# Performance work log

Measured on AMD Instinct MI355X. Metric: run time of the kernel, lower is better.

## Reference

```python
import jax, jax.numpy as jnp
import numpy as np

N = 100000
IN_DIM = 256
HID = 64
HEADS = 2
OUT_DIM = 64
E = 1600000
NEG_SLOPE = 0.2


def gat_conv(x, edge_index, W, att_src, att_dst, bias):
    # PyG GATConv with heads=HEADS, concat=True, add_self_loops=True.
    # x: [N, IN_DIM]; edge_index: [2, E] (row0=src, row1=dst)
    loops = jnp.arange(N, dtype=edge_index.dtype)
    src = jnp.concatenate([edge_index[0], loops])  # [E+N]
    dst = jnp.concatenate([edge_index[1], loops])  # [E+N]
    h = (x @ W).reshape(N, HEADS, HID)             # [N, H, C]
    a_src = jnp.einsum('nhc,hc->nh', h, att_src)   # [N, H]
    a_dst = jnp.einsum('nhc,hc->nh', h, att_dst)   # [N, H]
    e = jax.nn.leaky_relu(a_src[src] + a_dst[dst], NEG_SLOPE)  # [E+N, H]
    # segment softmax over incoming edges of each dst node
    m = jax.ops.segment_max(e, dst, num_segments=N)            # [N, H]
    p = jnp.exp(e - m[dst])
    denom = jax.ops.segment_sum(p, dst, num_segments=N)        # [N, H]
    alpha = p / denom[dst]                                     # [E+N, H]
    msg = h[src] * alpha[:, :, None]                           # [E+N, H, C]
    out = jax.ops.segment_sum(msg, dst, num_segments=N)        # [N, H, C]
    return out.reshape(N, HEADS * HID) + bias


def setup_inputs() -> dict:
    key = jax.random.key(0)
    ks = jax.random.split(key, 12)
    s_in = 1.0 / np.sqrt(IN_DIM)
    s_h = 1.0 / np.sqrt(HID)
    s_fc = 1.0 / np.sqrt(HEADS * HID * 2)
    return {
        'x': jax.random.normal(ks[0], (N, IN_DIM), jnp.float32),
        'edge_index_connected': jax.random.randint(ks[1], (2, E), 0, N, jnp.int32),
        'edge_index_liked': jax.random.randint(ks[2], (2, E), 0, N, jnp.int32),
        'W1': jax.random.normal(ks[3], (IN_DIM, HEADS * HID), jnp.float32) * s_in,
        'att_src1': jax.random.normal(ks[4], (HEADS, HID), jnp.float32) * s_h,
        'att_dst1': jax.random.normal(ks[5], (HEADS, HID), jnp.float32) * s_h,
        'b1': jnp.zeros((HEADS * HID,), jnp.float32),
        'W2': jax.random.normal(ks[6], (IN_DIM, HEADS * HID), jnp.float32) * s_in,
        'att_src2': jax.random.normal(ks[7], (HEADS, HID), jnp.float32) * s_h,
        'att_dst2': jax.random.normal(ks[8], (HEADS, HID), jnp.float32) * s_h,
        'b2': jnp.zeros((HEADS * HID,), jnp.float32),
        'fc_W': jax.random.normal(ks[9], (HEADS * HID * 2, OUT_DIM), jnp.float32) * s_fc,
        'fc_b': jnp.zeros((OUT_DIM,), jnp.float32),
    }


def reference(x, edge_index_connected, edge_index_liked, W1, att_src1, att_dst1, b1,
              W2, att_src2, att_dst2, b2, fc_W, fc_b):
    xc = jax.nn.relu(gat_conv(x, edge_index_connected, W1, att_src1, att_dst1, b1))
    xl = jax.nn.relu(gat_conv(x, edge_index_liked, W2, att_src2, att_dst2, b2))
    x_comb = jnp.concatenate([xc, xl], axis=1)  # [N, 4*HID]
    return x_comb @ fc_W + fc_b
```

## Files before the change

### kernel.cpp

```cpp
#include <hip/hip_runtime.h>
#include <hip/hip_fp16.h>
#include <math.h>

#define NN 100000
#define IN_DIM 256
#define HCH 128
#define OUT_DIM 64
#define EE 1600000
#define NEG_SLOPE 0.2f

#define NB 1024
#define NPB 98
#define CAP 2048

typedef _Float16 half8v __attribute__((ext_vector_type(8)));
typedef _Float16 half4v __attribute__((ext_vector_type(4)));
typedef _Float16 half2v __attribute__((ext_vector_type(2)));
typedef float float4v __attribute__((ext_vector_type(4)));

__device__ __forceinline__ float lrelu(float v) { return v > 0.f ? v : NEG_SLOPE * v; }

__global__ void convw_kernel(const float* __restrict__ W0, const float* __restrict__ W1,
                             const float* __restrict__ fcW,
                             _Float16* __restrict__ wt, _Float16* __restrict__ fcw16)
{
    int i = blockIdx.x * 256 + threadIdx.x;
    if (i < 2 * IN_DIM * HCH) {
        int l = i >> 15, rem = i & 32767;
        int c = rem >> 8, k = rem & 255;
        const float* W = l ? W1 : W0;
        wt[i] = (_Float16)W[(size_t)k * HCH + c];
        return;
    }
    int j = i - 2 * IN_DIM * HCH;
    if (j < 2 * HCH * OUT_DIM) {
        int l = j >> 13, rem = j & 8191;
        int c = rem >> 7, k = rem & 127;
        fcw16[j] = (_Float16)fcW[(size_t)(l * HCH + k) * OUT_DIM + c];
    }
}

__global__ __launch_bounds__(256, 5) void gemm_mfma(
    const float* __restrict__ x, const _Float16* __restrict__ wt,
    const float* __restrict__ att_src, const float* __restrict__ att_dst,
    _Float16* __restrict__ h16, float* __restrict__ a_s, float* __restrict__ a_d, int n)
{
    __shared__ _Float16 smem[64 * 72 + 128 * 72];
    __shared__ float attv[2][128];
    _Float16 (*As)[72] = (_Float16(*)[72])smem;
    _Float16 (*Bs)[72] = (_Float16(*)[72])(smem + 64 * 72);
    const int tid = threadIdx.x;
    const int lane = tid & 63, wave = tid >> 6;
    const int wm = wave & 1, wn = wave >> 1;
    const int q = lane >> 4, r16 = lane & 15;
    const int row0 = blockIdx.x * 64;

    if (tid < 128) { attv[0][tid] = att_src[tid]; attv[1][tid] = att_dst[tid]; }

    float4v acc[2][4];
#pragma unroll
    for (int i = 0; i < 2; ++i)
#pragma unroll
        for (int j = 0; j < 4; ++j) acc[i][j] = (float4v){0.f, 0.f, 0.f, 0.f};

    const int ar = tid >> 2, aq = tid & 3;
    const int br = tid >> 1, bh = tid & 1;
    const bool rok = (row0 + ar) < n;
    for (int kt = 0; kt < IN_DIM; kt += 64) {
        const float* xp = x + (size_t)(row0 + ar) * IN_DIM + kt + aq * 16;
#pragma unroll
        for (int i = 0; i < 4; ++i) {
            float4 v = rok ? *(const float4*)(xp + i * 4) : make_float4(0.f, 0.f, 0.f, 0.f);
            half4v hv = { (_Float16)v.x, (_Float16)v.y, (_Float16)v.z, (_Float16)v.w };
            *(half4v*)&As[ar][aq * 16 + i * 4] = hv;
        }
        const _Float16* wp = wt + (size_t)br * IN_DIM + kt + bh * 32;
#pragma unroll
        for (int i = 0; i < 4; ++i)
            *(half8v*)&Bs[br][bh * 32 + i * 8] = *(const half8v*)(wp + i * 8);
        __syncthreads();
#pragma unroll
        for (int s = 0; s < 2; ++s) {
            half8v af[2], bf[4];
#pragma unroll
            for (int t = 0; t < 2; ++t)
                af[t] = *(half8v*)&As[wm * 32 + t * 16 + r16][s * 32 + q * 8];
#pragma unroll
            for (int t = 0; t < 4; ++t)
                bf[t] = *(half8v*)&Bs[wn * 64 + t * 16 + r16][s * 32 + q * 8];
#pragma unroll
            for (int mt = 0; mt < 2; ++mt)
#pragma unroll
                for (int nt = 0; nt < 4; ++nt)
                    acc[mt][nt] = __builtin_amdgcn_mfma_f32_16x16x32_f16(
                        af[mt], bf[nt], acc[mt][nt], 0, 0, 0);
        }
        __syncthreads();
    }
    _Float16 (*eb)[136] = (_Float16(*)[136])smem;
#pragma unroll
    for (int mt = 0; mt < 2; ++mt) {
        const int er = wm * 32 + mt * 16 + q * 4;
#pragma unroll
        for (int reg = 0; reg < 4; ++reg)
#pragma unroll
            for (int nt = 0; nt < 4; ++nt)
                eb[er + reg][wn * 64 + nt * 16 + r16] = (_Float16)acc[mt][nt][reg];
    }
    __syncthreads();
    const int r = tid >> 1, hh = tid & 1;
    if (r < 64) {
        const int grow = row0 + r;
        if (grow < n) {
            float ds = 0.f, dd = 0.f;
#pragma unroll
            for (int i = 0; i < 8; ++i) {
                half8v v = *(half8v*)&eb[r][hh * 64 + i * 8];
                *(half8v*)(h16 + (size_t)grow * HCH + hh * 64 + i * 8) = v;
#pragma unroll
                for (int j = 0; j < 8; ++j) {
                    float f = (float)v[j];
                    ds = fmaf(f, attv[0][hh * 64 + i * 8 + j], ds);
                    dd = fmaf(f, attv[1][hh * 64 + i * 8 + j], dd);
                }
            }
            a_s[2 * grow + hh] = ds;
            a_d[2 * grow + hh] = dd;
        }
    }
}

__global__ __launch_bounds__(1024) void bucket_kernel(const int* __restrict__ src,
                                                      const int* __restrict__ dst,
                                                      int* __restrict__ gcursor,
                                                      int* __restrict__ bstore, int e)
{
    __shared__ int hist[NB];
    __shared__ int base[NB];
    const int tid = threadIdx.x;
    const int per = (e + gridDim.x - 1) / gridDim.x;
    const int e0 = blockIdx.x * per;
    const int e1 = min(e, e0 + per);
    for (int i = tid; i < NB; i += 1024) hist[i] = 0;
    __syncthreads();
    for (int i = e0 + tid; i < e1; i += 1024)
        atomicAdd(&hist[dst[i] / NPB], 1);
    __syncthreads();
    for (int b = tid; b < NB; b += 1024) {
        int c = hist[b];
        base[b] = c ? atomicAdd(&gcursor[b], c) : 0;
        hist[b] = 0;
    }
    __syncthreads();
    for (int i = e0 + tid; i < e1; i += 1024) {
        int d = dst[i];
        int s = src[i];
        int b = d / NPB;
        int pos = base[b] + atomicAdd(&hist[b], 1);
        if (pos >= 0 && pos < CAP) bstore[b * CAP + pos] = (s << 7) | (d - b * NPB);
    }
}

__global__ __launch_bounds__(256) void sort_kernel(
    const int* __restrict__ gcursor, int* __restrict__ bstore,
    int* __restrict__ gstart, int* __restrict__ gend, int n)
{
    __shared__ int raw[CAP];
    __shared__ int sorted[CAP];
    __shared__ int curs[128];
    __shared__ int scanbuf[128];
    const int tid = threadIdx.x;
    const int b = blockIdx.x;
    const int node0 = b * NPB;
    const int nnode = min(NPB, n - node0);
    if (nnode <= 0) return;
    int cnt = gcursor[b];
    cnt = cnt < 0 ? 0 : (cnt > CAP ? CAP : cnt);

    for (int i = tid; i < cnt; i += 256) raw[i] = bstore[b * CAP + i];
    if (tid < 128) curs[tid] = 0;
    __syncthreads();
    for (int i = tid; i < cnt; i += 256) atomicAdd(&curs[raw[i] & 127], 1);
    __syncthreads();
    if (tid < 128) scanbuf[tid] = curs[tid];
    __syncthreads();
    for (int off = 1; off < 128; off <<= 1) {
        int v = 0;
        if (tid < 128) { v = scanbuf[tid]; if (tid >= off) v += scanbuf[tid - off]; }
        __syncthreads();
        if (tid < 128) scanbuf[tid] = v;
        __syncthreads();
    }
    if (tid < 128) {
        int ex = tid ? scanbuf[tid - 1] : 0;
        curs[tid] = ex;
        if (tid < nnode) {
            gstart[node0 + tid] = b * CAP + ex;
            gend[node0 + tid] = b * CAP + scanbuf[tid];
        }
    }
    __syncthreads();
    for (int i = tid; i < cnt; i += 256) {
        int item = raw[i];
        int pos = atomicAdd(&curs[item & 127], 1);
        if (pos >= 0 && pos < CAP) sorted[pos] = item >> 7;
    }
    __syncthreads();
    for (int i = tid; i < cnt; i += 256) bstore[b * CAP + i] = sorted[i];
}

__global__ __launch_bounds__(256) void agg_kernel(
    const _Float16* __restrict__ h16, const float2* __restrict__ a_s,
    const float2* __restrict__ a_d, const int* __restrict__ gstart,
    const int* __restrict__ gend, const int* __restrict__ ssort,
    const float* __restrict__ bias, _Float16* __restrict__ xc16, int n)
{
    __shared__ float2 sh[4][2][64];
    const int wid = threadIdx.x >> 6, lane = threadIdx.x & 63;
    const int wbase = (blockIdx.x * 4 + wid) * 4;
    const float2* myhalf = &sh[wid][lane >> 5][0];
    const float b0 = bias[2 * lane], b1 = bias[2 * lane + 1];

    for (int ni = 0; ni < 4; ++ni) {
        const int node = wbase + ni;
        const bool valid = node < n;
        const int nn = valid ? node : 0;
        int start = gstart[nn], end = gend[nn];
        start = start < 0 ? 0 : (start > NB * CAP ? NB * CAP : start);
        end = end < start ? start : (end > NB * CAP ? NB * CAP : end);
        const float2 ad = a_d[nn];
        const float2 asn = a_s[nn];

        float acc0 = 0.f, acc1 = 0.f;
        float s0 = 0.f, s1 = 0.f;

        for (int base = start; base < end; base += 64) {
            const int j = base + lane;
            const int cnt = min(64, end - base);
            float p0 = 0.f, p1 = 0.f;
            int s = 0;
            if (j < end) {
                s = ssort[j];
                if ((unsigned)s >= (unsigned)n) s = 0;
                float2 a = a_s[s];
                p0 = __expf(lrelu(a.x + ad.x));
                p1 = __expf(lrelu(a.y + ad.y));
            }
            s0 += p0;
            s1 += p1;
            sh[wid][0][lane] = make_float2(__int_as_float(s), p0);
            sh[wid][1][lane] = make_float2(__int_as_float(s), p1);
            __builtin_amdgcn_wave_barrier();
            int t = 0;
            for (; t + 2 <= cnt; t += 2) {
                const float2 e0 = myhalf[t];
                const float2 e1 = myhalf[t + 1];
                const half2v hv0 =
                    *(const half2v*)(h16 + (size_t)__float_as_int(e0.x) * HCH + 2 * lane);
                const half2v hv1 =
                    *(const half2v*)(h16 + (size_t)__float_as_int(e1.x) * HCH + 2 * lane);
                acc0 = fmaf(e0.y, (float)hv0[0], acc0);
                acc1 = fmaf(e0.y, (float)hv0[1], acc1);
                acc0 = fmaf(e1.y, (float)hv1[0], acc0);
                acc1 = fmaf(e1.y, (float)hv1[1], acc1);
            }
            if (t < cnt) {
                const float2 e0 = myhalf[t];
                const half2v hv0 =
                    *(const half2v*)(h16 + (size_t)__float_as_int(e0.x) * HCH + 2 * lane);
                acc0 = fmaf(e0.y, (float)hv0[0], acc0);
                acc1 = fmaf(e0.y, (float)hv0[1], acc1);
            }
            __builtin_amdgcn_wave_barrier();
        }
        {
            const float ps0 = __expf(lrelu(asn.x + ad.x));
            const float ps1 = __expf(lrelu(asn.y + ad.y));
            const half2v hv = *(const half2v*)(h16 + (size_t)nn * HCH + 2 * lane);
            const float pl = (lane < 32) ? ps0 : ps1;
            acc0 = fmaf(pl, (float)hv[0], acc0);
            acc1 = fmaf(pl, (float)hv[1], acc1);
            if (lane == 0) { s0 += ps0; s1 += ps1; }
        }
#pragma unroll
        for (int m = 32; m >= 1; m >>= 1) {
            s0 += __shfl_xor(s0, m, 64);
            s1 += __shfl_xor(s1, m, 64);
        }
        const float dl = (lane < 32) ? s0 : s1;
        if (valid) {
            const float o0 = fmaxf(acc0 / dl + b0, 0.f);
            const float o1 = fmaxf(acc1 / dl + b1, 0.f);
            half2v o = { (_Float16)o0, (_Float16)o1 };
            *(half2v*)(xc16 + (size_t)node * HCH + 2 * lane) = o;
        }
    }
}

__global__ __launch_bounds__(256) void fc_mfma(const _Float16* __restrict__ xc16,
                                               const _Float16* __restrict__ fw16,
                                               const float* __restrict__ fcb,
                                               float* __restrict__ out, int n, int beta)
{
    __shared__ _Float16 axs[64][136];
    const int tid = threadIdx.x;
    const int lane = tid & 63, wave = tid >> 6;
    const int q = lane >> 4, r16 = lane & 15;
    const int row0 = blockIdx.x * 64;

#pragma unroll
    for (int i = 0; i < 4; ++i) {
        const int idx = i * 256 + tid;
        const int row = idx >> 4;
        const int kg = (idx & 15) * 8;
        half8v v = { 0, 0, 0, 0, 0, 0, 0, 0 };
        if (row0 + row < n)
            v = *(const half8v*)(xc16 + (size_t)(row0 + row) * HCH + kg);
        *(half8v*)&axs[row][kg] = v;
    }
    __syncthreads();

    float4v acc[4];
#pragma unroll
    for (int i = 0; i < 4; ++i) acc[i] = (float4v){0.f, 0.f, 0.f, 0.f};
#pragma unroll
    for (int s = 0; s < 4; ++s) {
        const half8v af = *(half8v*)&axs[wave * 16 + r16][s * 32 + q * 8];
#pragma unroll
        for (int nt = 0; nt < 4; ++nt) {
            const half8v bf =
                *(const half8v*)(fw16 + (size_t)(nt * 16 + r16) * HCH + s * 32 + q * 8);
            acc[nt] = __builtin_amdgcn_mfma_f32_16x16x32_f16(af, bf, acc[nt], 0, 0, 0);
        }
    }
#pragma unroll
    for (int nt = 0; nt < 4; ++nt) {
        const int col = nt * 16 + r16;
#pragma unroll
        for (int reg = 0; reg < 4; ++reg) {
            const int row = row0 + wave * 16 + q * 4 + reg;
            if (row < n) {
                float v = acc[nt][reg];
                if (beta) v += out[(size_t)row * OUT_DIM + col];
                else v += fcb[col];
                out[(size_t)row * OUT_DIM + col] = v;
            }
        }
    }
}

extern "C" void kernel_launch(void* const* d_in, const int* in_sizes, int n_in,
                              void* d_out, int out_size, void* d_ws, size_t ws_size,
                              hipStream_t stream)
{
    const float* x = (const float*)d_in[0];
    const int* ei[2] = { (const int*)d_in[1], (const int*)d_in[2] };
    const float* W[2] = { (const float*)d_in[3], (const float*)d_in[7] };
    const float* attS[2] = { (const float*)d_in[4], (const float*)d_in[8] };
    const float* attD[2] = { (const float*)d_in[5], (const float*)d_in[9] };
    const float* bias[2] = { (const float*)d_in[6], (const float*)d_in[10] };
    const float* fcW = (const float*)d_in[11];
    const float* fcb = (const float*)d_in[12];
    float* out = (float*)d_out;

    char* p = (char*)d_ws;
    size_t need = 0;
    auto carve = [&](size_t bytes) {
        char* r = p;
        size_t b = (bytes + 255) & ~(size_t)255;
        p += b;
        need += b;
        return r;
    };
    _Float16* h16 = (_Float16*)carve((size_t)NN * HCH * 2);
    _Float16* xc16 = (_Float16*)carve((size_t)NN * HCH * 2);
    _Float16* wt = (_Float16*)carve((size_t)2 * IN_DIM * HCH * 2);
    _Float16* fcw16 = (_Float16*)carve((size_t)2 * HCH * OUT_DIM * 2);
    float* a_s = (float*)carve((size_t)NN * 8);
    float* a_d = (float*)carve((size_t)NN * 8);
    int* gcursor = (int*)carve((size_t)NB * 4);
    int* bstore = (int*)carve((size_t)NB * CAP * 4);
    int* gstart = (int*)carve((size_t)NN * 4);
    int* gend = (int*)carve((size_t)NN * 4);
    if (need > ws_size) return;

    const int gemm_blocks = (NN + 63) / 64;
    const int agg_blocks = (NN + 15) / 16;
    const int conv_total = 2 * IN_DIM * HCH + 2 * HCH * OUT_DIM;

    convw_kernel<<<(conv_total + 255) / 256, 256, 0, stream>>>(W[0], W[1], fcW, wt, fcw16);

    for (int layer = 0; layer < 2; ++layer) {
        gemm_mfma<<<gemm_blocks, 256, 0, stream>>>(x, wt + (size_t)layer * IN_DIM * HCH,
                                                   attS[layer], attD[layer],
                                                   h16, a_s, a_d, NN);
        hipMemsetAsync(gcursor, 0, (size_t)NB * 4, stream);
        bucket_kernel<<<256, 1024, 0, stream>>>(ei[layer], ei[layer] + EE, gcursor, bstore, EE);
        sort_kernel<<<NB, 256, 0, stream>>>(gcursor, bstore, gstart, gend, NN);
        agg_kernel<<<agg_blocks, 256, 0, stream>>>(h16, (const float2*)a_s, (const float2*)a_d,
                                                   gstart, gend, bstore, bias[layer],
                                                   xc16, NN);
        fc_mfma<<<gemm_blocks, 256, 0, stream>>>(xc16, fcw16 + (size_t)layer * HCH * OUT_DIM,
                                                 fcb, out, NN, layer);
    }
}
```

Before: 531.3 us.

## Fuse both layers' projection GEMMs and widen aggregation gathers to 16-byte loads

The two per-layer x@W GEMMs become one launch that computes all 256 output columns, so x is read and converted once, and h16 and the attention scores are stored per layer. The aggregation kernel now has each 16-lane group handle one edge with 8-wide half loads, four edges per step, then sums the partial results with cross-lane shuffles. This reduces x traffic and the number of narrow gather instructions. In exchange the GEMM uses more registers and LDS (occupancy hint lowered from 5 to 3), and h16 storage doubles.

```diff
diff --git a/kernel.cpp b/kernel.cpp
--- a/kernel.cpp
+++ b/kernel.cpp
@@ -40,13 +40,14 @@
     }
 }
 
-__global__ __launch_bounds__(256, 5) void gemm_mfma(
+__global__ __launch_bounds__(256, 3) void gemm_mfma(
     const float* __restrict__ x, const _Float16* __restrict__ wt,
-    const float* __restrict__ att_src, const float* __restrict__ att_dst,
+    const float* __restrict__ attS0, const float* __restrict__ attD0,
+    const float* __restrict__ attS1, const float* __restrict__ attD1,
     _Float16* __restrict__ h16, float* __restrict__ a_s, float* __restrict__ a_d, int n)
 {
-    __shared__ _Float16 smem[64 * 72 + 128 * 72];
-    __shared__ float attv[2][128];
+    __shared__ _Float16 smem[64 * 72 + 256 * 72];
+    __shared__ float attv[4][128];
     _Float16 (*As)[72] = (_Float16(*)[72])smem;
     _Float16 (*Bs)[72] = (_Float16(*)[72])(smem + 64 * 72);
     const int tid = threadIdx.x;
@@ -55,16 +56,18 @@
     const int q = lane >> 4, r16 = lane & 15;
     const int row0 = blockIdx.x * 64;
 
-    if (tid < 128) { attv[0][tid] = att_src[tid]; attv[1][tid] = att_dst[tid]; }
-
-    float4v acc[2][4];
+    if (tid < 128) {
+        attv[0][tid] = attS0[tid]; attv[1][tid] = attD0[tid];
+        attv[2][tid] = attS1[tid]; attv[3][tid] = attD1[tid];
+    }
+
+    float4v acc[2][8];
 #pragma unroll
     for (int i = 0; i < 2; ++i)
 #pragma unroll
-        for (int j = 0; j < 4; ++j) acc[i][j] = (float4v){0.f, 0.f, 0.f, 0.f};
+        for (int j = 0; j < 8; ++j) acc[i][j] = (float4v){0.f, 0.f, 0.f, 0.f};
 
     const int ar = tid >> 2, aq = tid & 3;
-    const int br = tid >> 1, bh = tid & 1;
     const bool rok = (row0 + ar) < n;
     for (int kt = 0; kt < IN_DIM; kt += 64) {
         const float* xp = x + (size_t)(row0 + ar) * IN_DIM + kt + aq * 16;
@@ -74,59 +77,62 @@
             half4v hv = { (_Float16)v.x, (_Float16)v.y, (_Float16)v.z, (_Float16)v.w };
             *(half4v*)&As[ar][aq * 16 + i * 4] = hv;
         }
-        const _Float16* wp = wt + (size_t)br * IN_DIM + kt + bh * 32;
-#pragma unroll
-        for (int i = 0; i < 4; ++i)
-            *(half8v*)&Bs[br][bh * 32 + i * 8] = *(const half8v*)(wp + i * 8);
+        const _Float16* wp = wt + (size_t)tid * IN_DIM + kt;
+#pragma unroll
+        for (int i = 0; i < 8; ++i)
+            *(half8v*)&Bs[tid][i * 8] = *(const half8v*)(wp + i * 8);
         __syncthreads();
 #pragma unroll
         for (int s = 0; s < 2; ++s) {
-            half8v af[2], bf[4];
+            half8v af[2], bf[8];
 #pragma unroll
             for (int t = 0; t < 2; ++t)
                 af[t] = *(half8v*)&As[wm * 32 + t * 16 + r16][s * 32 + q * 8];
 #pragma unroll
-            for (int t = 0; t < 4; ++t)
-                bf[t] = *(half8v*)&Bs[wn * 64 + t * 16 + r16][s * 32 + q * 8];
+            for (int t = 0; t < 8; ++t)
+                bf[t] = *(half8v*)&Bs[wn * 128 + t * 16 + r16][s * 32 + q * 8];
 #pragma unroll
             for (int mt = 0; mt < 2; ++mt)
 #pragma unroll
-                for (int nt = 0; nt < 4; ++nt)
+                for (int nt = 0; nt < 8; ++nt)
                     acc[mt][nt] = __builtin_amdgcn_mfma_f32_16x16x32_f16(
                         af[mt], bf[nt], acc[mt][nt], 0, 0, 0);
         }
         __syncthreads();
     }
-    _Float16 (*eb)[136] = (_Float16(*)[136])smem;
+    _Float16 (*eb)[264] = (_Float16(*)[264])smem;
 #pragma unroll
     for (int mt = 0; mt < 2; ++mt) {
         const int er = wm * 32 + mt * 16 + q * 4;
 #pragma unroll
         for (int reg = 0; reg < 4; ++reg)
 #pragma unroll
-            for (int nt = 0; nt < 4; ++nt)
-                eb[er + reg][wn * 64 + nt * 16 + r16] = (_Float16)acc[mt][nt][reg];
-    }
-    __syncthreads();
-    const int r = tid >> 1, hh = tid & 1;
-    if (r < 64) {
-        const int grow = row0 + r;
-        if (grow < n) {
-            float ds = 0.f, dd = 0.f;
-#pragma unroll
-            for (int i = 0; i < 8; ++i) {
-                half8v v = *(half8v*)&eb[r][hh * 64 + i * 8];
-                *(half8v*)(h16 + (size_t)grow * HCH + hh * 64 + i * 8) = v;
-#pragma unroll
-                for (int j = 0; j < 8; ++j) {
-                    float f = (float)v[j];
-                    ds = fmaf(f, attv[0][hh * 64 + i * 8 + j], ds);
-                    dd = fmaf(f, attv[1][hh * 64 + i * 8 + j], dd);
-                }
+            for (int nt = 0; nt < 8; ++nt)
+                eb[er + reg][wn * 128 + nt * 16 + r16] = (_Float16)acc[mt][nt][reg];
+    }
+    __syncthreads();
+    const int r = tid >> 2, qq = tid & 3;
+    const int grow = row0 + r;
+    if (grow < n) {
+        const int l2 = qq >> 1;
+        const int hh = qq & 1;
+        const float* avS = &attv[l2 * 2 + 0][hh * 64];
+        const float* avD = &attv[l2 * 2 + 1][hh * 64];
+        _Float16* hout = h16 + (size_t)l2 * NN * HCH + (size_t)grow * HCH + hh * 64;
+        float ds = 0.f, dd = 0.f;
+#pragma unroll
+        for (int i = 0; i < 8; ++i) {
+            half8v v = *(half8v*)&eb[r][qq * 64 + i * 8];
+            *(half8v*)(hout + i * 8) = v;
+#pragma unroll
+            for (int j = 0; j < 8; ++j) {
+                float f = (float)v[j];
+                ds = fmaf(f, avS[i * 8 + j], ds);
+                dd = fmaf(f, avD[i * 8 + j], dd);
             }
-            a_s[2 * grow + hh] = ds;
-            a_d[2 * grow + hh] = dd;
-        }
+        }
+        a_s[(size_t)l2 * 2 * NN + 2 * grow + hh] = ds;
+        a_d[(size_t)l2 * 2 * NN + 2 * grow + hh] = dd;
     }
 }
 
@@ -218,8 +224,14 @@
     __shared__ float2 sh[4][2][64];
     const int wid = threadIdx.x >> 6, lane = threadIdx.x & 63;
     const int wbase = (blockIdx.x * 4 + wid) * 4;
-    const float2* myhalf = &sh[wid][lane >> 5][0];
-    const float b0 = bias[2 * lane], b1 = bias[2 * lane + 1];
+    const int cl = lane & 15;
+    const int w  = lane >> 4;
+    const int hh = cl >> 3;
+    const float2* myh = &sh[wid][hh][0];
+
+    float bv[8];
+#pragma unroll
+    for (int j = 0; j < 8; ++j) bv[j] = bias[cl * 8 + j];
 
     for (int ni = 0; ni < 4; ++ni) {
         const int node = wbase + ni;
@@ -231,7 +243,7 @@
         const float2 ad = a_d[nn];
         const float2 asn = a_s[nn];
 
-        float acc0 = 0.f, acc1 = 0.f;
+        float acc[8] = {0.f, 0.f, 0.f, 0.f, 0.f, 0.f, 0.f, 0.f};
         float s0 = 0.f, s1 = 0.f;
 
         for (int base = start; base < end; base += 64) {
@@ -251,48 +263,44 @@
             sh[wid][0][lane] = make_float2(__int_as_float(s), p0);
             sh[wid][1][lane] = make_float2(__int_as_float(s), p1);
             __builtin_amdgcn_wave_barrier();
-            int t = 0;
-            for (; t + 2 <= cnt; t += 2) {
-                const float2 e0 = myhalf[t];
-                const float2 e1 = myhalf[t + 1];
-                const half2v hv0 =
-                    *(const half2v*)(h16 + (size_t)__float_as_int(e0.x) * HCH + 2 * lane);
-                const half2v hv1 =
-                    *(const half2v*)(h16 + (size_t)__float_as_int(e1.x) * HCH + 2 * lane);
-                acc0 = fmaf(e0.y, (float)hv0[0], acc0);
-                acc1 = fmaf(e0.y, (float)hv0[1], acc1);
-                acc0 = fmaf(e1.y, (float)hv1[0], acc0);
-                acc1 = fmaf(e1.y, (float)hv1[1], acc1);
-            }
-            if (t < cnt) {
-                const float2 e0 = myhalf[t];
-                const half2v hv0 =
-                    *(const half2v*)(h16 + (size_t)__float_as_int(e0.x) * HCH + 2 * lane);
-                acc0 = fmaf(e0.y, (float)hv0[0], acc0);
-                acc1 = fmaf(e0.y, (float)hv0[1], acc1);
+            const int cnt4 = (cnt + 3) & ~3;
+            for (int t = 0; t < cnt4; t += 4) {
+                const float2 e = myh[t + w];
+                const half8v hv = *(const half8v*)(
+                    h16 + (size_t)__float_as_int(e.x) * HCH + cl * 8);
+#pragma unroll
+                for (int j2 = 0; j2 < 8; ++j2)
+                    acc[j2] = fmaf(e.y, (float)hv[j2], acc[j2]);
             }
             __builtin_amdgcn_wave_barrier();
         }
-        {
-            const float ps0 = __expf(lrelu(asn.x + ad.x));
-            const float ps1 = __expf(lrelu(asn.y + ad.y));
-            const half2v hv = *(const half2v*)(h16 + (size_t)nn * HCH + 2 * lane);
-            const float pl = (lane < 32) ? ps0 : ps1;
-            acc0 = fmaf(pl, (float)hv[0], acc0);
-            acc1 = fmaf(pl, (float)hv[1], acc1);
-            if (lane == 0) { s0 += ps0; s1 += ps1; }
+        const float ps0 = __expf(lrelu(asn.x + ad.x));
+        const float ps1 = __expf(lrelu(asn.y + ad.y));
+        if (w == 0) {
+            const half8v hv = *(const half8v*)(h16 + (size_t)nn * HCH + cl * 8);
+            const float pl = hh ? ps1 : ps0;
+#pragma unroll
+            for (int j2 = 0; j2 < 8; ++j2)
+                acc[j2] = fmaf(pl, (float)hv[j2], acc[j2]);
+        }
+        if (lane == 0) { s0 += ps0; s1 += ps1; }
+#pragma unroll
+        for (int j2 = 0; j2 < 8; ++j2) {
+            acc[j2] += __shfl_xor(acc[j2], 16, 64);
+            acc[j2] += __shfl_xor(acc[j2], 32, 64);
         }
 #pragma unroll
         for (int m = 32; m >= 1; m >>= 1) {
             s0 += __shfl_xor(s0, m, 64);
             s1 += __shfl_xor(s1, m, 64);
         }
-        const float dl = (lane < 32) ? s0 : s1;
-        if (valid) {
-            const float o0 = fmaxf(acc0 / dl + b0, 0.f);
-            const float o1 = fmaxf(acc1 / dl + b1, 0.f);
-            half2v o = { (_Float16)o0, (_Float16)o1 };
-            *(half2v*)(xc16 + (size_t)node * HCH + 2 * lane) = o;
+        if (valid && lane < 16) {
+            const float inv = 1.f / (hh ? s1 : s0);
+            half8v o;
+#pragma unroll
+            for (int j2 = 0; j2 < 8; ++j2)
+                o[j2] = (_Float16)fmaxf(acc[j2] * inv + bv[j2], 0.f);
+            *(half8v*)(xc16 + (size_t)node * HCH + cl * 8) = o;
         }
     }
 }
@@ -372,12 +380,12 @@
         need += b;
         return r;
     };
-    _Float16* h16 = (_Float16*)carve((size_t)NN * HCH * 2);
+    _Float16* h16 = (_Float16*)carve((size_t)2 * NN * HCH * 2);
     _Float16* xc16 = (_Float16*)carve((size_t)NN * HCH * 2);
     _Float16* wt = (_Float16*)carve((size_t)2 * IN_DIM * HCH * 2);
     _Float16* fcw16 = (_Float16*)carve((size_t)2 * HCH * OUT_DIM * 2);
-    float* a_s = (float*)carve((size_t)NN * 8);
-    float* a_d = (float*)carve((size_t)NN * 8);
+    float* a_s = (float*)carve((size_t)2 * NN * 8);
+    float* a_d = (float*)carve((size_t)2 * NN * 8);
     int* gcursor = (int*)carve((size_t)NB * 4);
     int* bstore = (int*)carve((size_t)NB * CAP * 4);
     int* gstart = (int*)carve((size_t)NN * 4);
@@ -390,16 +398,18 @@
 
     convw_kernel<<<(conv_total + 255) / 256, 256, 0, stream>>>(W[0], W[1], fcW, wt, fcw16);
 
+    gemm_mfma<<<gemm_blocks, 256, 0, stream>>>(x, wt, attS[0], attD[0], attS[1], attD[1],
+                                               h16, a_s, a_d, NN);
+
     for (int layer = 0; layer < 2; ++layer) {
-        gemm_mfma<<<gemm_blocks, 256, 0, stream>>>(x, wt + (size_t)layer * IN_DIM * HCH,
-                                                   attS[layer], attD[layer],
-                                                   h16, a_s, a_d, NN);
         hipMemsetAsync(gcursor, 0, (size_t)NB * 4, stream);
         bucket_kernel<<<256, 1024, 0, stream>>>(ei[layer], ei[layer] + EE, gcursor, bstore, EE);
         sort_kernel<<<NB, 256, 0, stream>>>(gcursor, bstore, gstart, gend, NN);
-        agg_kernel<<<agg_blocks, 256, 0, stream>>>(h16, (const float2*)a_s, (const float2*)a_d,
-                                                   gstart, gend, bstore, bias[layer],
-                                                   xc16, NN);
+        agg_kernel<<<agg_blocks, 256, 0, stream>>>(
+            h16 + (size_t)layer * NN * HCH,
+            (const float2*)a_s + (size_t)layer * NN,
+            (const float2*)a_d + (size_t)layer * NN,
+            gstart, gend, bstore, bias[layer], xc16, NN);
         fc_mfma<<<gemm_blocks, 256, 0, stream>>>(xc16, fcw16 + (size_t)layer * HCH * OUT_DIM,
                                                  fcb, out, NN, layer);
     }
```

New measurement: 498.5 us. 1.07x faster.
